# Performance work log

Measured on AMD Instinct MI355X. Metric: run time of the kernel, lower is better.

Reference implementation:

```python
import jax, jax.numpy as jnp
import numpy as np

N = 50000        # nodes
E = 1_600_000    # edges (avg degree 32)
H = 4            # attention heads
DPH = 32         # dims per head
D = H * DPH      # hidden/output dim = 128
IN_DIM = 5
NEG_SLOPE = 0.2
LN_EPS = 1e-5


def _glorot(key, shape):
    fan_in = shape[0] if len(shape) > 1 else shape[-1]
    return jax.random.normal(key, shape, jnp.float32) / jnp.sqrt(jnp.float32(fan_in))


def setup_inputs() -> dict:
    key = jax.random.key(0)
    ks = jax.random.split(key, 24)
    inp = {
        'x': jax.random.normal(ks[0], (N, IN_DIM), jnp.float32),
        'w_in': _glorot(ks[1], (IN_DIM, D)),
        'b_in': jnp.zeros((D,), jnp.float32),
    }
    for i in range(3):
        k = 2 + 6 * i
        inp[f'w{i}'] = _glorot(ks[k], (D, D))            # GAT linear
        inp[f'asrc{i}'] = _glorot(ks[k + 1], (H, DPH))   # att_src
        inp[f'adst{i}'] = _glorot(ks[k + 2], (H, DPH))   # att_dst
        inp[f'cb{i}'] = jnp.zeros((D,), jnp.float32)     # conv bias
        inp[f'g{i}'] = jnp.ones((D,), jnp.float32)       # LN gamma
        inp[f'lb{i}'] = jnp.zeros((D,), jnp.float32)     # LN beta
    inp['edge_index'] = jax.random.randint(ks[23], (2, E), 0, N, dtype=jnp.int32)
    return inp


def _gat_layer(h, src, dst, W, a_src, a_dst, bias):
    # h: [N, D]; src/dst: [E+N] (self loops included)
    xh = (h @ W).reshape(N, H, DPH)                      # [N, H, DPH]
    al_s = jnp.einsum('nhd,hd->nh', xh, a_src)           # [N, H]
    al_d = jnp.einsum('nhd,hd->nh', xh, a_dst)
    e = jax.nn.leaky_relu(al_s[src] + al_d[dst], NEG_SLOPE)   # [E', H]
    m = jax.ops.segment_max(e, dst, num_segments=N)      # segment softmax over incoming edges
    ex = jnp.exp(e - m[dst])
    denom = jax.ops.segment_sum(ex, dst, num_segments=N)
    alpha = ex / (denom[dst] + 1e-16)                    # [E', H]
    out = jax.ops.segment_sum(xh[src] * alpha[..., None], dst, num_segments=N)
    return out.reshape(N, D) + bias


def _layer_norm(x, g, b):
    mu = jnp.mean(x, axis=-1, keepdims=True)
    var = jnp.mean((x - mu) ** 2, axis=-1, keepdims=True)
    return (x - mu) * jax.lax.rsqrt(var + LN_EPS) * g + b


def reference(x, w_in, b_in,
              w0, asrc0, adst0, cb0, g0, lb0,
              w1, asrc1, adst1, cb1, g1, lb1,
              w2, asrc2, adst2, cb2, g2, lb2,
              edge_index):
    loops = jnp.arange(N, dtype=edge_index.dtype)
    src = jnp.concatenate([edge_index[0], loops])        # PyG GATConv add_self_loops=True
    dst = jnp.concatenate([edge_index[1], loops])
    h = x @ w_in + b_in                                  # [N, D]
    layers = [(w0, asrc0, adst0, cb0, g0, lb0),
              (w1, asrc1, adst1, cb1, g1, lb1),
              (w2, asrc2, adst2, cb2, g2, lb2)]
    for i, (W, a_s, a_d, cb, g, lb) in enumerate(layers):
        h_new = _gat_layer(h, src, dst, W, a_s, a_d, cb)
        h_new = _layer_norm(h_new, g, lb)
        if i < 2:
            h_new = jax.nn.relu(h_new)                   # dropout = identity in eval
        h = h + h_new                                    # dims always match (128)
    return h
```

## Files before the change

### kernel.cpp

```cpp
#include <hip/hip_runtime.h>

#define NN 50000
#define NE 1600000
#define EP (NE + NN)
#define D 128
#define H 4
#define NEG 0.2f
#define LN_EPS 1e-5f
#define NBUCK 49
#define BCAP 40960
#define BCAPC 49152
#define CHUNK 4096

typedef _Float16 f16;
typedef _Float16 half8 __attribute__((ext_vector_type(8)));
typedef _Float16 half2v __attribute__((ext_vector_type(2)));
typedef float f32x4v __attribute__((ext_vector_type(4)));
typedef unsigned short u16;
typedef unsigned int u32;

static __device__ __forceinline__ float leakyf(float v) { return fmaxf(v, NEG * v); }

static __device__ __forceinline__ int fkey(float v) {
    int b = __float_as_int(v);
    return b >= 0 ? b : (b ^ 0x7fffffff);
}
static __device__ __forceinline__ float fdec(int k) {
    return __int_as_float(k >= 0 ? k : (k ^ 0x7fffffff));
}
#define NEG_INF_KEY 0x807fffff

__global__ void k_init(int* __restrict__ gcur, int* __restrict__ gmaxk) {
    int t = threadIdx.x;
    if (t < NBUCK) gcur[t] = 0;
    if (t < 12) gmaxk[t] = NEG_INF_KEY;
}

#define BIN_BLKS 403
#define WT_BLKS 192
#define WS_BLKS 24
#define KIN_BLKS 3125
__global__ __launch_bounds__(256) void k_binfat(
        const int* __restrict__ ei, int* __restrict__ gcur, u32* __restrict__ binned,
        const float* __restrict__ w0, const float* __restrict__ w1,
        const float* __restrict__ w2, f16* __restrict__ wt,
        const float* __restrict__ as0, const float* __restrict__ ad0,
        const float* __restrict__ as1, const float* __restrict__ ad1,
        const float* __restrict__ as2, const float* __restrict__ ad2,
        f16* __restrict__ ws16,
        const float* __restrict__ x, const float* __restrict__ w_in,
        const float* __restrict__ b_in, f16* __restrict__ h16) {
    __shared__ u32 pk[CHUNK];
    __shared__ int hist[NBUCK], base[NBUCK], lcur[NBUCK];
    int tid = threadIdx.x;
    int bid = blockIdx.x;

    if (bid < BIN_BLKS) {
        int cbase = bid * CHUNK;
        if (tid < NBUCK) hist[tid] = 0;
        __syncthreads();
#pragma unroll
        for (int j = 0; j < CHUNK / 256; j++) {
            int k = cbase + j * 256 + tid;
            u32 v = 0xFFFFFFFFu;
            if (k < EP) {
                int src, dst;
                if (k < NE) { src = ei[k]; dst = ei[NE + k]; }
                else        { src = k - NE; dst = src; }
                v = ((u32)dst << 16) | (u32)src;
                atomicAdd(&hist[dst >> 10], 1);
            }
            pk[j * 256 + tid] = v;
        }
        __syncthreads();
        if (tid < NBUCK) {
            base[tid] = atomicAdd(&gcur[tid], hist[tid]);
            lcur[tid] = 0;
        }
        __syncthreads();
#pragma unroll
        for (int j = 0; j < CHUNK / 256; j++) {
            u32 v = pk[j * 256 + tid];
            if (v != 0xFFFFFFFFu) {
                int b = v >> 26;
                int pos = base[b] + atomicAdd(&lcur[b], 1);
                binned[(size_t)b * BCAP + pos] = v;
            }
        }
        return;
    }
    if (bid < BIN_BLKS + WT_BLKS) {
        int u = (bid - BIN_BLKS) * 256 + tid;
        int l = u / (D * D), rem = u % (D * D);
        int k = rem >> 7, c = rem & 127;
        const float* w = (l == 0) ? w0 : (l == 1) ? w1 : w2;
        wt[l * D * D + c * D + k] = (f16)w[rem];
        return;
    }
    if (bid < BIN_BLKS + WT_BLKS + WS_BLKS) {
        int v = (bid - BIN_BLKS - WT_BLKS) * 256 + tid;
        int l = v / (16 * D), rem = v % (16 * D);
        int c = rem >> 7, k = rem & 127;
        f16 out = (f16)0.f;
        if (c < 8) {
            int head = c >> 1;
            const float* w = (l == 0) ? w0 : (l == 1) ? w1 : w2;
            const float* av = (c & 1) ? ((l == 0) ? ad0 : (l == 1) ? ad1 : ad2)
                                      : ((l == 0) ? as0 : (l == 1) ? as1 : as2);
            float s = 0.f;
#pragma unroll
            for (int j = 0; j < 32; j++)
                s = fmaf(w[k * D + head * 32 + j], av[head * 32 + j], s);
            out = (f16)s;
        }
        ws16[l * 16 * D + c * D + k] = out;
        return;
    }
    int gid = (bid - BIN_BLKS - WT_BLKS - WS_BLKS) * 256 + tid;
    int n = gid >> 4;
    int d0 = (gid & 15) << 3;
    const float* xr = x + n * 5;
    float x0 = xr[0], x1 = xr[1], x2 = xr[2], x3 = xr[3], x4 = xr[4];
    half8 hv;
#pragma unroll
    for (int j = 0; j < 8; j++) {
        int d = d0 + j;
        float acc = b_in[d];
        acc = fmaf(x0, w_in[0 * D + d], acc);
        acc = fmaf(x1, w_in[1 * D + d], acc);
        acc = fmaf(x2, w_in[2 * D + d], acc);
        acc = fmaf(x3, w_in[3 * D + d], acc);
        acc = fmaf(x4, w_in[4 * D + d], acc);
        hv[j] = (f16)acc;
    }
    *(half8*)&h16[(size_t)n * D + d0] = hv;
}

__global__ __launch_bounds__(1024) void k_build(const int* __restrict__ gcur,
                                                const u32* __restrict__ binned,
                                                int2* __restrict__ rps,
                                                u16* __restrict__ csr) {
    __shared__ int hist[1024];
    __shared__ int sm[1024];
    int tid = threadIdx.x;
    int b = blockIdx.x;
    hist[tid] = 0;
    __syncthreads();
    int cnt = gcur[b];
    const u32* bb = binned + (size_t)b * BCAP;
    for (int i = tid; i < cnt; i += 1024)
        atomicAdd(&hist[(bb[i] >> 16) & 1023], 1);
    __syncthreads();
    int d = hist[tid];
    int pd = (d + 7) & ~7;
    sm[tid] = pd;
    __syncthreads();
    for (int off = 1; off < 1024; off <<= 1) {
        int t = (tid >= off) ? sm[tid - off] : 0;
        __syncthreads();
        sm[tid] += t;
        __syncthreads();
    }
    int basep = b * BCAPC + sm[tid] - pd;
    int node = (b << 10) + tid;
    if (node < NN) rps[node] = make_int2(basep, basep + pd);
    for (int j = d; j < pd; ++j) csr[basep + j] = 0xFFFFu;
    __syncthreads();
    hist[tid] = basep;
    __syncthreads();
    for (int i = tid; i < cnt; i += 1024) {
        u32 v = bb[i];
        int pos = atomicAdd(&hist[(v >> 16) & 1023], 1);
        csr[pos] = (u16)(v & 0xFFFFu);
    }
}

__global__ __launch_bounds__(256) void k_gemm(const f16* __restrict__ h16,
                                              const f16* __restrict__ wt,
                                              const f16* __restrict__ ws16,
                                              f16* __restrict__ xh,
                                              float* __restrict__ als,
                                              float* __restrict__ ald,
                                              int* __restrict__ gmaxk) {
    __shared__ int sgk[4];
    if (threadIdx.x < 4) sgk[threadIdx.x] = NEG_INF_KEY;
    int wid = threadIdx.x >> 6;
    int lane = threadIdx.x & 63;
    int wbase = blockIdx.x * 128 + wid * 32;
    int r = lane & 15;
    int g = lane >> 4;

    int arow0 = wbase + r;      if (arow0 >= NN) arow0 = NN - 1;
    int arow1 = wbase + 16 + r; if (arow1 >= NN) arow1 = NN - 1;
    const f16* a0p = h16 + (size_t)arow0 * D + g * 8;
    const f16* a1p = h16 + (size_t)arow1 * D + g * 8;

    f32x4v acc0[8], acc1[8], al0, al1;
#pragma unroll
    for (int nt = 0; nt < 8; nt++) {
        acc0[nt] = (f32x4v){0.f, 0.f, 0.f, 0.f};
        acc1[nt] = (f32x4v){0.f, 0.f, 0.f, 0.f};
    }
    al0 = (f32x4v){0.f, 0.f, 0.f, 0.f};
    al1 = (f32x4v){0.f, 0.f, 0.f, 0.f};

#pragma unroll
    for (int ks = 0; ks < 4; ks++) {
        half8 a0 = *(const half8*)(a0p + ks * 32);
        half8 a1 = *(const half8*)(a1p + ks * 32);
        half8 bal = *(const half8*)(ws16 + (size_t)r * D + ks * 32 + g * 8);
        al0 = __builtin_amdgcn_mfma_f32_16x16x32_f16(a0, bal, al0, 0, 0, 0);
        al1 = __builtin_amdgcn_mfma_f32_16x16x32_f16(a1, bal, al1, 0, 0, 0);
#pragma unroll
        for (int nt = 0; nt < 8; nt++) {
            half8 b = *(const half8*)(wt + (size_t)(nt * 16 + r) * D + ks * 32 + g * 8);
            acc0[nt] = __builtin_amdgcn_mfma_f32_16x16x32_f16(a0, b, acc0[nt], 0, 0, 0);
            acc1[nt] = __builtin_amdgcn_mfma_f32_16x16x32_f16(a1, b, acc1[nt], 0, 0, 0);
        }
    }

#pragma unroll
    for (int rg = 0; rg < 4; rg++) {
        int n0 = wbase + g * 4 + rg;
        if (n0 < NN) {
#pragma unroll
            for (int nt = 0; nt < 8; nt++)
                xh[(size_t)n0 * D + nt * 16 + r] = (f16)acc0[nt][rg];
        }
        int n1 = wbase + 16 + g * 4 + rg;
        if (n1 < NN) {
#pragma unroll
            for (int nt = 0; nt < 8; nt++)
                xh[(size_t)n1 * D + nt * 16 + r] = (f16)acc1[nt][rg];
        }
    }

    float m = -1e30f;
#pragma unroll
    for (int rg = 0; rg < 4; rg++) {
        int n0 = wbase + g * 4 + rg;
        int n1 = wbase + 16 + g * 4 + rg;
        float v0 = al0[rg], v1 = al1[rg];
        if (r < 8) {
            int hh = r >> 1;
            if (r & 1) {
                if (n0 < NN) ald[n0 * H + hh] = v0;
                if (n1 < NN) ald[n1 * H + hh] = v1;
            } else {
                if (n0 < NN) als[n0 * H + hh] = v0;
                if (n1 < NN) als[n1 * H + hh] = v1;
                m = fmaxf(m, fmaxf(v0, v1));
            }
        }
    }
    m = fmaxf(m, __shfl_xor(m, 16));
    m = fmaxf(m, __shfl_xor(m, 32));
    __syncthreads();
    if (lane < 8 && !(r & 1)) atomicMax(&sgk[r >> 1], fkey(m));
    __syncthreads();
    if (threadIdx.x < 4) atomicMax(&gmaxk[threadIdx.x], sgk[threadIdx.x]);
}

__global__ __launch_bounds__(256) void k_agg(const f16* __restrict__ xh,
                                             const float* __restrict__ als,
                                             const float* __restrict__ ald,
                                             const int* __restrict__ gmaxk,
                                             const int2* __restrict__ rps,
                                             const u16* __restrict__ csr,
                                             const float* __restrict__ cb,
                                             const float* __restrict__ gamma,
                                             const float* __restrict__ beta,
                                             f16* __restrict__ h16,
                                             float* __restrict__ hout, int do_relu) {
    int node = blockIdx.x * 4 + (threadIdx.x >> 6);
    if (node >= NN) return;
    int lane = threadIdx.x & 63;
    int slot = lane >> 4;
    int q = lane & 15;
    int head = q >> 2;
    unsigned qo = q * 8;

    int2 se = rps[node];
    int start = se.x, end = se.y;

    float adH = ald[node * H + head];
    float mH = leakyf(fdec(gmaxk[head]) + adH);

    float acc[8];
#pragma unroll
    for (int j = 0; j < 8; j++) acc[j] = 0.f;
    float den = 0.f;

    int sh = (slot & 1) << 4;
    bool hiw = (slot & 2) != 0;

    for (int e = start; e < end; e += 8) {
        uint4 cw = *(const uint4*)(csr + e);
        unsigned dw0 = hiw ? cw.y : cw.x;
        unsigned dw1 = hiw ? cw.w : cw.z;
        unsigned s0 = (dw0 >> sh) & 0xffffu;
        unsigned s1 = (dw1 >> sh) & 0xffffu;
        bool v0 = s0 != 0xffffu;
        bool v1 = s1 != 0xffffu;
        unsigned sc0 = v0 ? s0 : 0u;
        unsigned sc1 = v1 ? s1 : 0u;
        float al0 = als[sc0 * 4u + (unsigned)head];
        float al1 = als[sc1 * 4u + (unsigned)head];
        float ev0 = v0 ? __expf(leakyf(al0 + adH) - mH) : 0.f;
        float ev1 = v1 ? __expf(leakyf(al1 + adH) - mH) : 0.f;
        den += ev0 + ev1;
        half8 p0 = *(const half8*)(xh + sc0 * 128u + qo);
        half8 p1 = *(const half8*)(xh + sc1 * 128u + qo);
#pragma unroll
        for (int j = 0; j < 8; j++)
            acc[j] = fmaf(ev0, (float)p0[j], fmaf(ev1, (float)p1[j], acc[j]));
    }

    den += __shfl_xor(den, 16);
    den += __shfl_xor(den, 32);
#pragma unroll
    for (int j = 0; j < 8; j++) {
        acc[j] += __shfl_xor(acc[j], 16);
        acc[j] += __shfl_xor(acc[j], 32);
    }

    float inv_den = 1.f / (den + 1e-16f);
    float o[8];
    const float4* cb4 = (const float4*)(cb + q * 8);
    float4 cba = cb4[0], cbb = cb4[1];
    o[0] = fmaf(acc[0], inv_den, cba.x);
    o[1] = fmaf(acc[1], inv_den, cba.y);
    o[2] = fmaf(acc[2], inv_den, cba.z);
    o[3] = fmaf(acc[3], inv_den, cba.w);
    o[4] = fmaf(acc[4], inv_den, cbb.x);
    o[5] = fmaf(acc[5], inv_den, cbb.y);
    o[6] = fmaf(acc[6], inv_den, cbb.z);
    o[7] = fmaf(acc[7], inv_den, cbb.w);

    float s = 0.f;
#pragma unroll
    for (int j = 0; j < 8; j++) s += o[j];
#pragma unroll
    for (int off = 1; off < 16; off <<= 1) s += __shfl_xor(s, off);
    float mean = s * (1.f / 128.f);
    float v = 0.f;
    float c[8];
#pragma unroll
    for (int j = 0; j < 8; j++) { c[j] = o[j] - mean; v = fmaf(c[j], c[j], v); }
#pragma unroll
    for (int off = 1; off < 16; off <<= 1) v += __shfl_xor(v, off);
    float inv = rsqrtf(v * (1.f / 128.f) + LN_EPS);

    int dim = q * 8 + slot * 2;
    float2 g2 = *(const float2*)(gamma + dim);
    float2 b2 = *(const float2*)(beta + dim);
    float r0 = c[slot * 2] * inv * g2.x + b2.x;
    float r1 = c[slot * 2 + 1] * inv * g2.y + b2.y;
    if (do_relu) { r0 = fmaxf(r0, 0.f); r1 = fmaxf(r1, 0.f); }
    half2v hv16 = *(const half2v*)&h16[(size_t)node * D + dim];
    float n0 = (float)hv16[0] + r0;
    float n1 = (float)hv16[1] + r1;
    if (do_relu) {
        half2v h2; h2[0] = (f16)n0; h2[1] = (f16)n1;
        *(half2v*)&h16[(size_t)node * D + dim] = h2;
    } else {
        *(float2*)&hout[(size_t)node * D + dim] = (float2){n0, n1};
    }
}

extern "C" void kernel_launch(void* const* d_in, const int* in_sizes, int n_in,
                              void* d_out, int out_size, void* d_ws, size_t ws_size,
                              hipStream_t stream) {
    const float* x    = (const float*)d_in[0];
    const float* w_in = (const float*)d_in[1];
    const float* b_in = (const float*)d_in[2];
    const int*   ei   = (const int*)d_in[21];
    float* hout = (float*)d_out;

    char* w = (char*)d_ws;
    int* gmaxk  = (int*)w;   w += 64;
    int* gcur   = (int*)w;   w += 256;
    int2* rps   = (int2*)w;  w += (size_t)NN * 8;
    u16* csr    = (u16*)w;   w += (size_t)NBUCK * BCAPC * 2;
    f16* h16    = (f16*)w;   w += (size_t)NN * D * 2;
    f16* xh     = (f16*)w;   w += (size_t)NN * D * 2;
    f16* wt     = (f16*)w;   w += (size_t)3 * D * D * 2;
    f16* ws16   = (f16*)w;   w += (size_t)3 * 16 * D * 2;
    float* als  = (float*)w; w += (size_t)NN * H * 4;
    float* ald  = (float*)w; w += (size_t)NN * H * 4;
    u32* binned = (u32*)xh;

    k_init<<<1, 64, 0, stream>>>(gcur, gmaxk);
    k_binfat<<<BIN_BLKS + WT_BLKS + WS_BLKS + KIN_BLKS, 256, 0, stream>>>(
        ei, gcur, binned,
        (const float*)d_in[3], (const float*)d_in[9], (const float*)d_in[15], wt,
        (const float*)d_in[4], (const float*)d_in[5],
        (const float*)d_in[10], (const float*)d_in[11],
        (const float*)d_in[16], (const float*)d_in[17], ws16,
        x, w_in, b_in, h16);
    k_build<<<NBUCK, 1024, 0, stream>>>(gcur, binned, rps, csr);

    for (int L = 0; L < 3; ++L) {
        const float* cb   = (const float*)d_in[6 + 6 * L];
        const float* g    = (const float*)d_in[7 + 6 * L];
        const float* lb   = (const float*)d_in[8 + 6 * L];
        k_gemm<<<(NN + 127) / 128, 256, 0, stream>>>(h16, wt + (size_t)L * D * D,
                                                     ws16 + (size_t)L * 16 * D,
                                                     xh, als, ald, gmaxk + 4 * L);
        k_agg<<<(NN + 3) / 4, 256, 0, stream>>>(xh, als, ald, gmaxk + 4 * L, rps, csr,
                                                cb, g, lb, h16, hout, L < 2 ? 1 : 0);
    }
}
```

Measured before the change: 359.4 us.

## Software-pipeline aggregation gathers and replace init kernel with memset

The edge loop in the aggregation kernel is double-buffered: CSR indices, attention logits and feature rows for the next group of 8 edges are loaded before the current group's exp and FMA work runs, so gather latency can overlap compute. The max-key encoding becomes an unsigned order-preserving key whose minimum is zero, which lets the init kernel be replaced by a hipMemsetAsync on the workspace header. The prefetch raises register pressure in the aggregation kernel, which may lower occupancy.

```diff
diff --git a/kernel.cpp b/kernel.cpp
--- a/kernel.cpp
+++ b/kernel.cpp
@@ -21,19 +21,12 @@
 
 static __device__ __forceinline__ float leakyf(float v) { return fmaxf(v, NEG * v); }
 
-static __device__ __forceinline__ int fkey(float v) {
+static __device__ __forceinline__ u32 ukey(float v) {
     int b = __float_as_int(v);
-    return b >= 0 ? b : (b ^ 0x7fffffff);
-}
-static __device__ __forceinline__ float fdec(int k) {
-    return __int_as_float(k >= 0 ? k : (k ^ 0x7fffffff));
-}
-#define NEG_INF_KEY 0x807fffff
-
-__global__ void k_init(int* __restrict__ gcur, int* __restrict__ gmaxk) {
-    int t = threadIdx.x;
-    if (t < NBUCK) gcur[t] = 0;
-    if (t < 12) gmaxk[t] = NEG_INF_KEY;
+    return (u32)(b >= 0 ? (b | 0x80000000) : ~b);
+}
+static __device__ __forceinline__ float udec(u32 u) {
+    return __int_as_float((u & 0x80000000u) ? (int)(u & 0x7fffffffu) : ~(int)u);
 }
 
 #define BIN_BLKS 403
@@ -181,9 +174,9 @@
                                               f16* __restrict__ xh,
                                               float* __restrict__ als,
                                               float* __restrict__ ald,
-                                              int* __restrict__ gmaxk) {
-    __shared__ int sgk[4];
-    if (threadIdx.x < 4) sgk[threadIdx.x] = NEG_INF_KEY;
+                                              u32* __restrict__ gmaxk) {
+    __shared__ u32 sgk[4];
+    if (threadIdx.x < 4) sgk[threadIdx.x] = 0u;
     int wid = threadIdx.x >> 6;
     int lane = threadIdx.x & 63;
     int wbase = blockIdx.x * 128 + wid * 32;
@@ -256,7 +249,7 @@
     m = fmaxf(m, __shfl_xor(m, 16));
     m = fmaxf(m, __shfl_xor(m, 32));
     __syncthreads();
-    if (lane < 8 && !(r & 1)) atomicMax(&sgk[r >> 1], fkey(m));
+    if (lane < 8 && !(r & 1)) atomicMax(&sgk[r >> 1], ukey(m));
     __syncthreads();
     if (threadIdx.x < 4) atomicMax(&gmaxk[threadIdx.x], sgk[threadIdx.x]);
 }
@@ -264,7 +257,7 @@
 __global__ __launch_bounds__(256) void k_agg(const f16* __restrict__ xh,
                                              const float* __restrict__ als,
                                              const float* __restrict__ ald,
-                                             const int* __restrict__ gmaxk,
+                                             const u32* __restrict__ gmaxk,
                                              const int2* __restrict__ rps,
                                              const u16* __restrict__ csr,
                                              const float* __restrict__ cb,
@@ -284,7 +277,7 @@
     int start = se.x, end = se.y;
 
     float adH = ald[node * H + head];
-    float mH = leakyf(fdec(gmaxk[head]) + adH);
+    float mH = leakyf(udec(gmaxk[head]) + adH);
 
     float acc[8];
 #pragma unroll
@@ -294,27 +287,52 @@
     int sh = (slot & 1) << 4;
     bool hiw = (slot & 2) != 0;
 
-    for (int e = start; e < end; e += 8) {
-        uint4 cw = *(const uint4*)(csr + e);
-        unsigned dw0 = hiw ? cw.y : cw.x;
-        unsigned dw1 = hiw ? cw.w : cw.z;
-        unsigned s0 = (dw0 >> sh) & 0xffffu;
-        unsigned s1 = (dw1 >> sh) & 0xffffu;
-        bool v0 = s0 != 0xffffu;
-        bool v1 = s1 != 0xffffu;
-        unsigned sc0 = v0 ? s0 : 0u;
-        unsigned sc1 = v1 ? s1 : 0u;
-        float al0 = als[sc0 * 4u + (unsigned)head];
-        float al1 = als[sc1 * 4u + (unsigned)head];
-        float ev0 = v0 ? __expf(leakyf(al0 + adH) - mH) : 0.f;
-        float ev1 = v1 ? __expf(leakyf(al1 + adH) - mH) : 0.f;
-        den += ev0 + ev1;
-        half8 p0 = *(const half8*)(xh + sc0 * 128u + qo);
-        half8 p1 = *(const half8*)(xh + sc1 * 128u + qo);
-#pragma unroll
-        for (int j = 0; j < 8; j++)
-            acc[j] = fmaf(ev0, (float)p0[j], fmaf(ev1, (float)p1[j], acc[j]));
-    }
+    bool v0A, v1A, v0B, v1B;
+    float al0A, al1A, al0B, al1B;
+    half8 p0A, p1A, p0B, p1B;
+
+#define LOADG(S, E)                                                           \
+    {                                                                         \
+        uint4 cw = *(const uint4*)(csr + (E));                                \
+        unsigned dw0 = hiw ? cw.y : cw.x;                                     \
+        unsigned dw1 = hiw ? cw.w : cw.z;                                     \
+        unsigned s0 = (dw0 >> sh) & 0xffffu;                                  \
+        unsigned s1 = (dw1 >> sh) & 0xffffu;                                  \
+        v0##S = s0 != 0xffffu;                                                \
+        v1##S = s1 != 0xffffu;                                                \
+        unsigned sc0 = v0##S ? s0 : 0u;                                       \
+        unsigned sc1 = v1##S ? s1 : 0u;                                       \
+        al0##S = als[sc0 * 4u + (unsigned)head];                              \
+        al1##S = als[sc1 * 4u + (unsigned)head];                              \
+        p0##S = *(const half8*)(xh + sc0 * 128u + qo);                        \
+        p1##S = *(const half8*)(xh + sc1 * 128u + qo);                        \
+    }
+
+#define CONSUME(S)                                                            \
+    {                                                                         \
+        float ev0 = v0##S ? __expf(leakyf(al0##S + adH) - mH) : 0.f;          \
+        float ev1 = v1##S ? __expf(leakyf(al1##S + adH) - mH) : 0.f;          \
+        den += ev0 + ev1;                                                     \
+        _Pragma("unroll")                                                     \
+        for (int j = 0; j < 8; j++)                                           \
+            acc[j] = fmaf(ev0, (float)p0##S[j],                               \
+                          fmaf(ev1, (float)p1##S[j], acc[j]));                \
+    }
+
+    int n8 = (end - start) >> 3;
+    int e1 = start + 8;
+    LOADG(A, start)
+    int rem = n8;
+    while (rem >= 2) {
+        LOADG(B, e1) e1 += 8;
+        CONSUME(A)
+        if (rem >= 3) { LOADG(A, e1) e1 += 8; }
+        CONSUME(B)
+        rem -= 2;
+    }
+    if (rem & 1) CONSUME(A)
+#undef LOADG
+#undef CONSUME
 
     den += __shfl_xor(den, 16);
     den += __shfl_xor(den, 32);
@@ -378,7 +396,7 @@
     float* hout = (float*)d_out;
 
     char* w = (char*)d_ws;
-    int* gmaxk  = (int*)w;   w += 64;
+    u32* gmaxk  = (u32*)w;   w += 64;
     int* gcur   = (int*)w;   w += 256;
     int2* rps   = (int2*)w;  w += (size_t)NN * 8;
     u16* csr    = (u16*)w;   w += (size_t)NBUCK * BCAPC * 2;
@@ -390,7 +408,7 @@
     float* ald  = (float*)w; w += (size_t)NN * H * 4;
     u32* binned = (u32*)xh;
 
-    k_init<<<1, 64, 0, stream>>>(gcur, gmaxk);
+    hipMemsetAsync(d_ws, 0, 320, stream);
     k_binfat<<<BIN_BLKS + WT_BLKS + WS_BLKS + KIN_BLKS, 256, 0, stream>>>(
         ei, gcur, binned,
         (const float*)d_in[3], (const float*)d_in[9], (const float*)d_in[15], wt,
```

Result: faster. 350.1 us (-2.6%).
